# Kernel optimization log

Measured on AMD Instinct MI355X. Metric: run time of the kernel, lower is better.

## Reference

```python
import jax, jax.numpy as jnp
import numpy as np

B, N, M, K = 128, 20000, 85400, 3  # trajectories, variables, clauses, literals/clause


def setup_inputs() -> dict:
    key = jax.random.key(0)
    k_v, k_idx, k_sign, k_xs = jax.random.split(key, 4)
    v = jax.random.normal(k_v, (B, N), dtype=jnp.float32)
    input_idx = jax.random.randint(k_idx, (B, M, K), 0, N, dtype=jnp.int32)
    # literal signs are exactly +/-1
    input_sign = jnp.where(jax.random.normal(k_sign, (B, M, K)) > 0, 1.0, -1.0).astype(jnp.float32)
    xl = jnp.ones((B, M), dtype=jnp.float32)            # long-term memory (init 1)
    xs = jax.random.uniform(k_xs, (B, M), dtype=jnp.float32)  # short-term memory in [0,1]
    # [alpha, beta, gamma, delta, epsilon, zeta] -- typical MemComputing coefficients
    param = jnp.array([5.0, 20.0, 0.25, 0.05, 0.001, 0.1], dtype=jnp.float32)
    return {"v": v, "xl": xl, "xs": xs, "param": param,
            "input_sign": input_sign, "input_idx": input_idx}


def reference(v, xl, xs, param, input_sign, input_idx):
    """Faithful port of OR.calc_grad. Returns (C, grad_v, dxl, dxs)."""
    b = v.shape[0]
    k = input_idx.shape[-1]
    alpha, beta, gamma, delta, epsilon, zeta = param
    b_idx = jnp.arange(b)[:, None, None]                # (B,1,1)
    inp = v[b_idx, input_idx] * input_sign              # (B,M,K) gather + sign
    v_top, v_top_idx = jax.lax.top_k(inp, 2)            # top-2 literal values per clause
    v_top = (1.0 - v_top) * 0.5                         # transform; v_top[...,0] is smallest -> C
    C = v_top[..., 0]                                   # (B,M) clause 'distance to satisfied'
    hot = jax.nn.one_hot(v_top_idx[..., 0], k, dtype=v.dtype)  # (B,M,K) mask of max literal
    # G: C everywhere, second-best value at the max-literal slot, scaled by xl*xs
    G = jnp.where(hot > 0, v_top[..., 1:2], C[..., None]) * (xl * xs)[..., None]
    # R: C only at the max-literal slot, scaled by (1+zeta*xl)*(1-xs)
    R = hot * C[..., None] * ((1.0 + zeta * xl) * (1.0 - xs))[..., None]
    dv = -(G + R) * input_sign                          # (B,M,K)
    grad_v = jnp.zeros_like(v).at[b_idx, input_idx].add(dv)  # scatter-add over dim 1
    dxl = -alpha * (C - delta)                          # (B,M)
    dxs = -beta * (xs + epsilon) * (C - gamma)          # (B,M)
    return C, grad_v, dxl, dxs
```

## Files before the change

kernel.cpp:

```cpp
#include <hip/hip_runtime.h>


#define NMAX 20000
#define BPB  2

typedef int   int4v   __attribute__((ext_vector_type(4)));
typedef float float4v __attribute__((ext_vector_type(4)));

__device__ __forceinline__ void clause_math(
    float a0, float a1, float a2, float xlv, float xsv, float zeta,
    float& C, float& g0, float& g1, float& g2)
{
    int k0; float m0, m1;
    if (a0 >= a1) {
        if (a0 >= a2) { k0 = 0; m0 = a0; m1 = fmaxf(a1, a2); }
        else          { k0 = 2; m0 = a2; m1 = fmaxf(a0, a1); }
    } else {
        if (a1 >= a2) { k0 = 1; m0 = a1; m1 = fmaxf(a0, a2); }
        else          { k0 = 2; m0 = a2; m1 = fmaxf(a0, a1); }
    }
    C = (1.f - m0) * 0.5f;
    const float T2 = (1.f - m1) * 0.5f;
    const float gl = xlv * xsv;
    const float rC = C * ((1.f + zeta * xlv) * (1.f - xsv));
    g0 = (k0 == 0 ? T2 : C) * gl + (k0 == 0 ? rC : 0.f);
    g1 = (k0 == 1 ? T2 : C) * gl + (k0 == 1 ? rC : 0.f);
    g2 = (k0 == 2 ? T2 : C) * gl + (k0 == 2 ? rC : 0.f);
}

__global__ __launch_bounds__(1024, 4) void or_priv4(
    const float* __restrict__ v,
    const float* __restrict__ xl,
    const float* __restrict__ xs,
    const float* __restrict__ param,
    const float* __restrict__ sign,
    const int*   __restrict__ idx,
    float* __restrict__ outC,
    float* __restrict__ outdxl,
    float* __restrict__ outdxs,
    float* __restrict__ partial,
    int N, int M, int B, int chunk)
{
    __shared__ float sv[NMAX];
    __shared__ float sg[NMAX];

    const int id  = blockIdx.x;
    const int cpx = gridDim.x >> 3;
    const int cid = ((gridDim.x & 7) == 0) ? ((id & 7) * cpx + (id >> 3)) : id;
    const int b   = cid >> 1;
    const int j   = cid & 1;
    const int tid = threadIdx.x;

    {
        const float4v* __restrict__ v4 = (const float4v*)(v + (size_t)b * N);
        float4v* sv4 = (float4v*)sv;
        float4v* sg4 = (float4v*)sg;
        const int n4 = N >> 2;
        const float4v z = {0.f, 0.f, 0.f, 0.f};
        for (int i = tid; i < n4; i += 1024) {
            sv4[i] = v4[i];
            sg4[i] = z;
        }
        for (int i = (n4 << 2) + tid; i < N; i += 1024) {
            sv[i] = v[(size_t)b * N + i];
            sg[i] = 0.f;
        }
    }
    __syncthreads();

    const float alpha = param[0], beta = param[1], gamma = param[2];
    const float delta = param[3], eps  = param[4], zeta  = param[5];

    const int mstart = j * chunk;
    const int mend   = min(M, mstart + chunk);
    const int mlen   = mend - mstart;

    if (mlen > 0 && (mlen & 3) == 0) {
        const int ngroups = mlen >> 2;
        int g = tid;
        int4v   ia = {}, ib = {}, ic = {};
        float4v sa = {}, sb = {}, sc = {}, xl4 = {}, xs4 = {};
        if (g < ngroups) {
            const size_t base = (size_t)b * M + mstart + ((size_t)g << 2);
            const int4v*   __restrict__ ip = (const int4v*)(idx + base * 3);
            const float4v* __restrict__ sp = (const float4v*)(sign + base * 3);
            ia = __builtin_nontemporal_load(ip + 0);
            ib = __builtin_nontemporal_load(ip + 1);
            ic = __builtin_nontemporal_load(ip + 2);
            sa = __builtin_nontemporal_load(sp + 0);
            sb = __builtin_nontemporal_load(sp + 1);
            sc = __builtin_nontemporal_load(sp + 2);
            xl4 = __builtin_nontemporal_load((const float4v*)(xl + base));
            xs4 = __builtin_nontemporal_load((const float4v*)(xs + base));
        }
        for (; g < ngroups; g += 1024) {
            const int gn = g + 1024;
            int4v   ia2 = {}, ib2 = {}, ic2 = {};
            float4v sa2 = {}, sb2 = {}, sc2 = {}, xl42 = {}, xs42 = {};
            if (gn < ngroups) {
                const size_t basen = (size_t)b * M + mstart + ((size_t)gn << 2);
                const int4v*   __restrict__ ipn = (const int4v*)(idx + basen * 3);
                const float4v* __restrict__ spn = (const float4v*)(sign + basen * 3);
                ia2 = __builtin_nontemporal_load(ipn + 0);
                ib2 = __builtin_nontemporal_load(ipn + 1);
                ic2 = __builtin_nontemporal_load(ipn + 2);
                sa2 = __builtin_nontemporal_load(spn + 0);
                sb2 = __builtin_nontemporal_load(spn + 1);
                sc2 = __builtin_nontemporal_load(spn + 2);
                xl42 = __builtin_nontemporal_load((const float4v*)(xl + basen));
                xs42 = __builtin_nontemporal_load((const float4v*)(xs + basen));
            }

            const size_t base = (size_t)b * M + mstart + ((size_t)g << 2);
            const int   ii[12] = {ia.x, ia.y, ia.z, ia.w, ib.x, ib.y, ib.z, ib.w,
                                  ic.x, ic.y, ic.z, ic.w};
            const float ss[12] = {sa.x, sa.y, sa.z, sa.w, sb.x, sb.y, sb.z, sb.w,
                                  sc.x, sc.y, sc.z, sc.w};
            const float xlA[4] = {xl4.x, xl4.y, xl4.z, xl4.w};
            const float xsA[4] = {xs4.x, xs4.y, xs4.z, xs4.w};
            float Cv[4], dxlv[4], dxsv[4];

            #pragma unroll
            for (int c = 0; c < 4; ++c) {
                const int   i0 = ii[3*c], i1 = ii[3*c+1], i2 = ii[3*c+2];
                const float s0 = ss[3*c], s1 = ss[3*c+1], s2 = ss[3*c+2];
                const float a0 = sv[i0] * s0, a1 = sv[i1] * s1, a2 = sv[i2] * s2;
                float C, g0, g1, g2;
                clause_math(a0, a1, a2, xlA[c], xsA[c], zeta, C, g0, g1, g2);
                unsafeAtomicAdd(&sg[i0], -g0 * s0);
                unsafeAtomicAdd(&sg[i1], -g1 * s1);
                unsafeAtomicAdd(&sg[i2], -g2 * s2);
                Cv[c]   = C;
                dxlv[c] = -alpha * (C - delta);
                dxsv[c] = -beta * (xsA[c] + eps) * (C - gamma);
            }
            const float4v cv  = {Cv[0], Cv[1], Cv[2], Cv[3]};
            const float4v lv  = {dxlv[0], dxlv[1], dxlv[2], dxlv[3]};
            const float4v svo = {dxsv[0], dxsv[1], dxsv[2], dxsv[3]};
            __builtin_nontemporal_store(cv,  (float4v*)(outC + base));
            __builtin_nontemporal_store(lv,  (float4v*)(outdxl + base));
            __builtin_nontemporal_store(svo, (float4v*)(outdxs + base));

            ia = ia2; ib = ib2; ic = ic2;
            sa = sa2; sb = sb2; sc = sc2;
            xl4 = xl42; xs4 = xs42;
        }
    } else {
        for (int m = mstart + tid; m < mend; m += 1024) {
            const size_t bm  = (size_t)b * M + m;
            const size_t bm3 = bm * 3;
            const int   i0 = idx[bm3 + 0], i1 = idx[bm3 + 1], i2 = idx[bm3 + 2];
            const float s0 = sign[bm3 + 0], s1 = sign[bm3 + 1], s2 = sign[bm3 + 2];
            const float a0 = sv[i0] * s0, a1 = sv[i1] * s1, a2 = sv[i2] * s2;
            const float xlv = xl[bm], xsv = xs[bm];
            float C, g0, g1, g2;
            clause_math(a0, a1, a2, xlv, xsv, zeta, C, g0, g1, g2);
            unsafeAtomicAdd(&sg[i0], -g0 * s0);
            unsafeAtomicAdd(&sg[i1], -g1 * s1);
            unsafeAtomicAdd(&sg[i2], -g2 * s2);
            outC[bm]   = C;
            outdxl[bm] = -alpha * (C - delta);
            outdxs[bm] = -beta * (xsv + eps) * (C - gamma);
        }
    }
    __syncthreads();

    {
        float* __restrict__ pj = partial + ((size_t)j * B + b) * N;
        const float4v* sg4 = (const float4v*)sg;
        const int n4 = N >> 2;
        for (int i = tid; i < n4; i += 1024)
            ((float4v*)pj)[i] = sg4[i];
        for (int i = (n4 << 2) + tid; i < N; i += 1024) pj[i] = sg[i];
    }
}

__global__ __launch_bounds__(256) void reduce2(
    const float4v* __restrict__ p, float4v* __restrict__ out, int n4, int stride4)
{
    int i = blockIdx.x * 256 + threadIdx.x;
    const int gs = gridDim.x * 256;
    for (; i < n4; i += gs) {
        const float4v a = p[i];
        const float4v b = p[i + stride4];
        out[i] = a + b;
    }
}

__global__ __launch_bounds__(256) void zero_f4(float4v* __restrict__ p, int n4) {
    int i = blockIdx.x * blockDim.x + threadIdx.x;
    int stride = gridDim.x * blockDim.x;
    const float4v z = {0.f, 0.f, 0.f, 0.f};
    for (; i < n4; i += stride) p[i] = z;
}

__global__ __launch_bounds__(256) void or_kernel(
    const float* __restrict__ v, const float* __restrict__ xl,
    const float* __restrict__ xs, const float* __restrict__ param,
    const float* __restrict__ sign, const int* __restrict__ idx,
    float* __restrict__ outC, float* __restrict__ gradv,
    float* __restrict__ outdxl, float* __restrict__ outdxs, int N, int M)
{
    const int m = blockIdx.x * blockDim.x + threadIdx.x;
    const int b = blockIdx.y;
    if (m >= M) return;
    const size_t bm = (size_t)b * M + m;
    const size_t bm3 = bm * 3;
    const int   i0 = idx[bm3 + 0], i1 = idx[bm3 + 1], i2 = idx[bm3 + 2];
    const float s0 = sign[bm3 + 0], s1 = sign[bm3 + 1], s2 = sign[bm3 + 2];
    const float* __restrict__ vb = v + (size_t)b * N;
    const float a0 = vb[i0] * s0, a1 = vb[i1] * s1, a2 = vb[i2] * s2;
    const float xlv = xl[bm], xsv = xs[bm];
    const float alpha = param[0], beta = param[1], gamma = param[2];
    const float delta = param[3], eps  = param[4], zeta  = param[5];

    float C, g0, g1, g2;
    clause_math(a0, a1, a2, xlv, xsv, zeta, C, g0, g1, g2);

    float* __restrict__ gb = gradv + (size_t)b * N;
    atomicAdd(&gb[i0], -g0 * s0);
    atomicAdd(&gb[i1], -g1 * s1);
    atomicAdd(&gb[i2], -g2 * s2);

    outC[bm]   = C;
    outdxl[bm] = -alpha * (C - delta);
    outdxs[bm] = -beta * (xsv + eps) * (C - gamma);
}

extern "C" void kernel_launch(void* const* d_in, const int* in_sizes, int n_in,
                              void* d_out, int out_size, void* d_ws, size_t ws_size,
                              hipStream_t stream) {
    const float* v     = (const float*)d_in[0];
    const float* xl    = (const float*)d_in[1];
    const float* xs    = (const float*)d_in[2];
    const float* param = (const float*)d_in[3];
    const float* sign  = (const float*)d_in[4];
    const int*   idx   = (const int*)d_in[5];

    const int B = 128;
    const int N = in_sizes[0] / B;
    const int M = in_sizes[1] / B;

    float* outC   = (float*)d_out;
    float* gradv  = outC   + (size_t)in_sizes[1];
    float* outdxl = gradv  + (size_t)in_sizes[0];
    float* outdxs = outdxl + (size_t)in_sizes[1];

    const size_t bn = (size_t)B * N;
    const size_t ws_need = (size_t)BPB * bn * sizeof(float);

    if (N <= NMAX && ws_size >= ws_need && (bn % 4) == 0 && (M % 4) == 0) {
        float* partial = (float*)d_ws;
        const int chunk = (((M + BPB - 1) / BPB) + 3) & ~3;
        or_priv4<<<dim3(BPB * B), dim3(1024), 0, stream>>>(
            v, xl, xs, param, sign, idx, outC, outdxl, outdxs,
            (float*)partial, N, M, B, chunk);
        const int n4 = (int)(bn / 4);
        const int rblocks = min(2048, (n4 + 255) / 256);
        reduce2<<<dim3(rblocks), dim3(256), 0, stream>>>(
            (const float4v*)partial, (float4v*)gradv, n4, n4);
    } else {
        const int n4 = (int)(bn / 4);
        zero_f4<<<dim3((n4 + 255) / 256), dim3(256), 0, stream>>>((float4v*)gradv, n4);
        dim3 grid((M + 255) / 256, B);
        or_kernel<<<grid, dim3(256), 0, stream>>>(v, xl, xs, param, sign, idx,
                                                  outC, gradv, outdxl, outdxs, N, M);
    }
}
```

Measured before the change: 461.7 us.

## Replace LDS-private gradient accumulation with direct global atomics and drop reduce kernel

Removes the shared-memory gradient buffer and the partial-sum workspace plus its reduction kernel. Gradients are now scattered with hardware float atomics directly into the zeroed global output. Each batch row is split across four blocks, and the launch bound targets higher occupancy thanks to halved LDS use. This trades cheap LDS atomics and a small reduction pass for many L2 atomics with cross-block contention.

```diff
diff --git a/kernel.cpp b/kernel.cpp
--- a/kernel.cpp
+++ b/kernel.cpp
@@ -2,7 +2,7 @@
 
 
 #define NMAX 20000
-#define BPB  2
+#define BPB  4
 
 typedef int   int4v   __attribute__((ext_vector_type(4)));
 typedef float float4v __attribute__((ext_vector_type(4)));
@@ -28,7 +28,7 @@
     g2 = (k0 == 2 ? T2 : C) * gl + (k0 == 2 ? rC : 0.f);
 }
 
-__global__ __launch_bounds__(1024, 4) void or_priv4(
+__global__ __launch_bounds__(1024, 8) void or_priv5(
     const float* __restrict__ v,
     const float* __restrict__ xl,
     const float* __restrict__ xs,
@@ -38,38 +38,32 @@
     float* __restrict__ outC,
     float* __restrict__ outdxl,
     float* __restrict__ outdxs,
-    float* __restrict__ partial,
+    float* __restrict__ gradv,
     int N, int M, int B, int chunk)
 {
     __shared__ float sv[NMAX];
-    __shared__ float sg[NMAX];
 
     const int id  = blockIdx.x;
     const int cpx = gridDim.x >> 3;
     const int cid = ((gridDim.x & 7) == 0) ? ((id & 7) * cpx + (id >> 3)) : id;
-    const int b   = cid >> 1;
-    const int j   = cid & 1;
+    const int b   = cid >> 2;
+    const int j   = cid & 3;
     const int tid = threadIdx.x;
 
     {
         const float4v* __restrict__ v4 = (const float4v*)(v + (size_t)b * N);
         float4v* sv4 = (float4v*)sv;
-        float4v* sg4 = (float4v*)sg;
         const int n4 = N >> 2;
-        const float4v z = {0.f, 0.f, 0.f, 0.f};
-        for (int i = tid; i < n4; i += 1024) {
-            sv4[i] = v4[i];
-            sg4[i] = z;
-        }
-        for (int i = (n4 << 2) + tid; i < N; i += 1024) {
+        for (int i = tid; i < n4; i += 1024) sv4[i] = v4[i];
+        for (int i = (n4 << 2) + tid; i < N; i += 1024)
             sv[i] = v[(size_t)b * N + i];
-            sg[i] = 0.f;
-        }
     }
     __syncthreads();
 
     const float alpha = param[0], beta = param[1], gamma = param[2];
     const float delta = param[3], eps  = param[4], zeta  = param[5];
+
+    float* __restrict__ gb = gradv + (size_t)b * N;
 
     const int mstart = j * chunk;
     const int mend   = min(M, mstart + chunk);
@@ -127,9 +121,9 @@
                 const float a0 = sv[i0] * s0, a1 = sv[i1] * s1, a2 = sv[i2] * s2;
                 float C, g0, g1, g2;
                 clause_math(a0, a1, a2, xlA[c], xsA[c], zeta, C, g0, g1, g2);
-                unsafeAtomicAdd(&sg[i0], -g0 * s0);
-                unsafeAtomicAdd(&sg[i1], -g1 * s1);
-                unsafeAtomicAdd(&sg[i2], -g2 * s2);
+                unsafeAtomicAdd(&gb[i0], -g0 * s0);
+                unsafeAtomicAdd(&gb[i1], -g1 * s1);
+                unsafeAtomicAdd(&gb[i2], -g2 * s2);
                 Cv[c]   = C;
                 dxlv[c] = -alpha * (C - delta);
                 dxsv[c] = -beta * (xsA[c] + eps) * (C - gamma);
@@ -155,35 +149,13 @@
             const float xlv = xl[bm], xsv = xs[bm];
             float C, g0, g1, g2;
             clause_math(a0, a1, a2, xlv, xsv, zeta, C, g0, g1, g2);
-            unsafeAtomicAdd(&sg[i0], -g0 * s0);
-            unsafeAtomicAdd(&sg[i1], -g1 * s1);
-            unsafeAtomicAdd(&sg[i2], -g2 * s2);
+            unsafeAtomicAdd(&gb[i0], -g0 * s0);
+            unsafeAtomicAdd(&gb[i1], -g1 * s1);
+            unsafeAtomicAdd(&gb[i2], -g2 * s2);
             outC[bm]   = C;
             outdxl[bm] = -alpha * (C - delta);
             outdxs[bm] = -beta * (xsv + eps) * (C - gamma);
         }
-    }
-    __syncthreads();
-
-    {
-        float* __restrict__ pj = partial + ((size_t)j * B + b) * N;
-        const float4v* sg4 = (const float4v*)sg;
-        const int n4 = N >> 2;
-        for (int i = tid; i < n4; i += 1024)
-            ((float4v*)pj)[i] = sg4[i];
-        for (int i = (n4 << 2) + tid; i < N; i += 1024) pj[i] = sg[i];
-    }
-}
-
-__global__ __launch_bounds__(256) void reduce2(
-    const float4v* __restrict__ p, float4v* __restrict__ out, int n4, int stride4)
-{
-    int i = blockIdx.x * 256 + threadIdx.x;
-    const int gs = gridDim.x * 256;
-    for (; i < n4; i += gs) {
-        const float4v a = p[i];
-        const float4v b = p[i + stride4];
-        out[i] = a + b;
     }
 }
 
@@ -247,20 +219,16 @@
     float* outdxs = outdxl + (size_t)in_sizes[1];
 
     const size_t bn = (size_t)B * N;
-    const size_t ws_need = (size_t)BPB * bn * sizeof(float);
-
-    if (N <= NMAX && ws_size >= ws_need && (bn % 4) == 0 && (M % 4) == 0) {
-        float* partial = (float*)d_ws;
+    const int n4 = (int)(bn / 4);
+
+    if (N <= NMAX && (bn % 4) == 0 && (M % 4) == 0) {
+        zero_f4<<<dim3(min(2048, (n4 + 255) / 256)), dim3(256), 0, stream>>>(
+            (float4v*)gradv, n4);
         const int chunk = (((M + BPB - 1) / BPB) + 3) & ~3;
-        or_priv4<<<dim3(BPB * B), dim3(1024), 0, stream>>>(
+        or_priv5<<<dim3(BPB * B), dim3(1024), 0, stream>>>(
             v, xl, xs, param, sign, idx, outC, outdxl, outdxs,
-            (float*)partial, N, M, B, chunk);
-        const int n4 = (int)(bn / 4);
-        const int rblocks = min(2048, (n4 + 255) / 256);
-        reduce2<<<dim3(rblocks), dim3(256), 0, stream>>>(
-            (const float4v*)partial, (float4v*)gradv, n4, n4);
+            gradv, N, M, B, chunk);
     } else {
-        const int n4 = (int)(bn / 4);
         zero_f4<<<dim3((n4 + 255) / 256), dim3(256), 0, stream>>>((float4v*)gradv, n4);
         dim3 grid((M + 255) / 256, B);
         or_kernel<<<grid, dim3(256), 0, stream>>>(v, xl, xs, param, sign, idx,
```

Result: slower. 1.834 ms (+297.3%).
